# Performance work log

Hardware: AMD Instinct MI355X
Metric: run time of the kernel (lower is better)

The kernel has to match this reference:

```python
import jax, jax.numpy as jnp
import numpy as np

C = 16        # channel_n
HID = 128     # hidden width of 1x1 MLP
FIRE_RATE = 0.5
STEP_SIZE = 1.0
ALIVE_THRESH = 0.1
B, H, W = 16, 256, 256


def _perceive_kernel():
    # identity + Sobel filters, angle = 0.0 so cos=1, sin=0
    ident = np.outer([0.0, 1.0, 0.0], [0.0, 1.0, 0.0]).astype(np.float32)
    dxk = (np.outer([1.0, 2.0, 1.0], [-1.0, 0.0, 1.0]) / 8.0).astype(np.float32)
    dyk = dxk.T
    k3 = np.stack([ident, dxk, dyk], axis=-1)  # [3,3,3]
    # TF depthwise layout: out channel index = c*3 + k  -> tile over channels
    rhs = np.tile(k3, (1, 1, C)).reshape(3, 3, 1, 3 * C)  # HWIO, groups=C
    return jnp.asarray(rhs)


def _get_living_mask(x):
    alpha = x[:, :, :, 3:4]
    pooled = jax.lax.reduce_window(alpha, -jnp.inf, jax.lax.max,
                                   (1, 3, 3, 1), (1, 1, 1, 1), 'SAME')
    return pooled > ALIVE_THRESH


def _perceive(x):
    rhs = _perceive_kernel()
    return jax.lax.conv_general_dilated(
        x, rhs, window_strides=(1, 1), padding='SAME',
        dimension_numbers=('NHWC', 'HWIO', 'NHWC'),
        feature_group_count=C)  # [B,H,W,3C]


def setup_inputs() -> dict:
    key = jax.random.key(0)
    kx, kw1, kb1, ku = jax.random.split(key, 4)
    x = jax.random.normal(kx, (B, H, W, C), dtype=jnp.float32)
    # dmodel params: Conv2D(128,1,relu) then Conv2D(16,1,zeros init); use
    # random values for a meaningful numeric baseline
    W1 = jax.random.normal(kw1, (3 * C, HID), dtype=jnp.float32) * 0.1
    b1 = jax.random.normal(kb1, (HID,), dtype=jnp.float32) * 0.01
    W2 = jax.random.normal(jax.random.fold_in(key, 7), (HID, C), dtype=jnp.float32) * 0.1
    b2 = jnp.zeros((C,), dtype=jnp.float32)
    rand_u = jax.random.uniform(ku, (B, H, W, 1), dtype=jnp.float32)
    return {"x": x, "W1": W1, "b1": b1, "W2": W2, "b2": b2, "rand_u": rand_u}


def reference(x, W1, b1, W2, b2, rand_u):
    pre_life_mask = _get_living_mask(x)
    y = _perceive(x)                                         # [B,H,W,48]
    h = jax.nn.relu(jnp.einsum('bhwc,cd->bhwd', y, W1) + b1)  # [B,H,W,128]
    dx = (jnp.einsum('bhwd,dc->bhwc', h, W2) + b2) * STEP_SIZE
    update_mask = (rand_u <= FIRE_RATE).astype(x.dtype)
    x = x + dx * update_mask
    post_life_mask = _get_living_mask(x)
    life_mask = (pre_life_mask & post_life_mask).astype(x.dtype)
    return x * life_mask
```

## Files before the change

kernel.cpp:

```cpp
#include <hip/hip_runtime.h>


#define NC 16
#define NHID 128
#define NPIX (16 * 256 * 256)
#define MG 0.015f

typedef __attribute__((ext_vector_type(8))) short s8b;
typedef __attribute__((ext_vector_type(4))) float f4;

__device__ __forceinline__ unsigned short f2bf(float f) {
    union { float f; unsigned int u; } v; v.f = f;
    unsigned int r = (v.u + 0x7FFFu + ((v.u >> 16) & 1u)) >> 16;
    return (unsigned short)r;
}
__device__ __forceinline__ unsigned int pack2(float a, float b) {
    return (unsigned int)f2bf(a) | ((unsigned int)f2bf(b) << 16);
}

__global__ __launch_bounds__(256) void ca_prep(
    const float* __restrict__ W1, const float* __restrict__ b1,
    const float* __restrict__ W2, uint4* __restrict__ w1p, uint4* __restrict__ w2p)
{
    const int tid = threadIdx.x;
    if (blockIdx.x == 0) {
        for (int idx = tid; idx < 1024; idx += 256) {
            const int fid = idx >> 6, lane = idx & 63;
            const int k0 = fid >> 3, mt = fid & 7;
            const int q = lane >> 4, i = lane & 15;
            unsigned int u[4];
            #pragma unroll
            for (int jp = 0; jp < 4; ++jp) {
                int k = k0 * 32 + q * 8 + jp * 2;
                float v0 = (k < 48) ? W1[k * 128 + mt * 16 + i] : ((k == 48) ? b1[mt * 16 + i] : 0.f);
                k++;
                float v1 = (k < 48) ? W1[k * 128 + mt * 16 + i] : ((k == 48) ? b1[mt * 16 + i] : 0.f);
                u[jp] = pack2(v0, v1);
            }
            w1p[idx] = make_uint4(u[0], u[1], u[2], u[3]);
        }
    } else {
        for (int idx = tid; idx < 256; idx += 256) {
            const int k2 = idx >> 6, lane = idx & 63;
            const int q = lane >> 4, i = lane & 15;
            unsigned int u[4];
            #pragma unroll
            for (int jp = 0; jp < 4; ++jp) {
                const int k = k2 * 32 + q * 8 + jp * 2;
                u[jp] = pack2(W2[k * 16 + i], W2[(k + 1) * 16 + i]);
            }
            w2p[idx] = make_uint4(u[0], u[1], u[2], u[3]);
        }
    }
}

__global__ __launch_bounds__(256, 2) void ca_update(
    const float* __restrict__ x, const float* __restrict__ b2,
    const float* __restrict__ rand_u, const uint4* __restrict__ w1p,
    const uint4* __restrict__ w2p, float* __restrict__ out,
    float* __restrict__ ws_alpha, unsigned char* __restrict__ ws_pre)
{
    __shared__ __align__(16) float xt[18 * 18 * 20];
    __shared__ __align__(16) unsigned short yfs[4 * 2 * 528];
    __shared__ __align__(16) unsigned short hbs[4 * 16 * 136];
    __shared__ float lsr[256];

    const int tid  = threadIdx.x;
    const int lane = tid & 63;
    const int li   = lane & 15;
    const int lq   = lane >> 4;
    const int wv   = tid >> 6;
    const int tx   = tid & 15, ty = tid >> 4;
    const int w0 = blockIdx.x * 16, h0 = blockIdx.y * 16, bb = blockIdx.z;

    s8b w1f[2][8], w2f[4];
    const s8b* w1s = (const s8b*)w1p;
    const s8b* w2s = (const s8b*)w2p;
    #pragma unroll
    for (int k0 = 0; k0 < 2; ++k0)
        #pragma unroll
        for (int mt = 0; mt < 8; ++mt)
            w1f[k0][mt] = w1s[(k0 * 8 + mt) * 64 + lane];
    #pragma unroll
    for (int k2 = 0; k2 < 4; ++k2) w2f[k2] = w2s[k2 * 64 + lane];
    float b2v[4];
    #pragma unroll
    for (int r = 0; r < 4; ++r) b2v[r] = b2[lq * 4 + r];

    for (int i = tid; i < 324; i += 256) {
        const int ly = i / 18, lx = i - ly * 18;
        const int gh = h0 + ly - 1, gw = w0 + lx - 1;
        float4 v0, v1, v2, v3;
        if (gh >= 0 && gh < 256 && gw >= 0 && gw < 256) {
            const float4* p = (const float4*)(x + (((size_t)bb * 256 + gh) * 256 + gw) * NC);
            v0 = p[0]; v1 = p[1]; v2 = p[2]; v3 = p[3];
        } else {
            v0 = v1 = v2 = v3 = make_float4(0.f, 0.f, 0.f, 0.f);
        }
        float4* t = (float4*)(xt + i * 20);
        t[0] = v0; t[1] = v1; t[2] = v2; t[3] = v3;
    }
    const size_t gpix = ((size_t)bb * 256 + h0 + ty) * 256 + (w0 + tx);
    lsr[tid] = rand_u[gpix];
    __syncthreads();

    const int o_mm = ((ty + 0) * 18 + tx + 0) * 20, o_m0 = ((ty + 0) * 18 + tx + 1) * 20, o_mp = ((ty + 0) * 18 + tx + 2) * 20;
    const int o_0m = ((ty + 1) * 18 + tx + 0) * 20, o_cc = ((ty + 1) * 18 + tx + 1) * 20, o_0p = ((ty + 1) * 18 + tx + 2) * 20;
    const int o_pm = ((ty + 2) * 18 + tx + 0) * 20, o_p0 = ((ty + 2) * 18 + tx + 1) * 20, o_pp = ((ty + 2) * 18 + tx + 2) * 20;

    float am = xt[o_mm + 3];
    am = fmaxf(am, xt[o_m0 + 3]); am = fmaxf(am, xt[o_mp + 3]);
    am = fmaxf(am, xt[o_0m + 3]); am = fmaxf(am, xt[o_cc + 3]); am = fmaxf(am, xt[o_0p + 3]);
    am = fmaxf(am, xt[o_pm + 3]); am = fmaxf(am, xt[o_p0 + 3]); am = fmaxf(am, xt[o_pp + 3]);
    ws_pre[gpix] = (am > 0.1f) ? (unsigned char)1 : (unsigned char)0;

    unsigned int yu[24];
    #pragma unroll
    for (int cq = 0; cq < 4; ++cq) {
        const int co = cq * 4;
        float4 vmm = *(const float4*)(xt + o_mm + co); const float* pmm = (const float*)&vmm;
        float4 vm0 = *(const float4*)(xt + o_m0 + co); const float* pm0 = (const float*)&vm0;
        float4 vmp = *(const float4*)(xt + o_mp + co); const float* pmp = (const float*)&vmp;
        float4 v0m = *(const float4*)(xt + o_0m + co); const float* p0m = (const float*)&v0m;
        float4 vcc = *(const float4*)(xt + o_cc + co); const float* pcc = (const float*)&vcc;
        float4 v0p = *(const float4*)(xt + o_0p + co); const float* p0p = (const float*)&v0p;
        float4 vpm = *(const float4*)(xt + o_pm + co); const float* ppm = (const float*)&vpm;
        float4 vp0 = *(const float4*)(xt + o_p0 + co); const float* pp0 = (const float*)&vp0;
        float4 vpp = *(const float4*)(xt + o_pp + co); const float* ppp = (const float*)&vpp;
        float yl[12];
        #pragma unroll
        for (int cc = 0; cc < 4; ++cc) {
            const float xmm = pmm[cc], xm0 = pm0[cc], xmp = pmp[cc];
            const float x0m = p0m[cc], xcc = pcc[cc], x0p = p0p[cc];
            const float xpm = ppm[cc], xp0 = pp0[cc], xpp = ppp[cc];
            yl[cc * 3 + 0] = xcc;
            yl[cc * 3 + 1] = ((xmp - xmm) + 2.f * (x0p - x0m) + (xpp - xpm)) * 0.125f;
            yl[cc * 3 + 2] = ((xpm - xmm) + 2.f * (xp0 - xm0) + (xpp - xmp)) * 0.125f;
        }
        #pragma unroll
        for (int m2 = 0; m2 < 6; ++m2) yu[cq * 6 + m2] = pack2(yl[2 * m2], yl[2 * m2 + 1]);
    }

    unsigned short* yfw = yfs + wv * (2 * 528);
    unsigned short* hbw = hbs + wv * (16 * 136);

    for (int s = 0; s < 4; ++s) {
        const int t = wv * 4 + s;
        if ((ty & 3) == s) {
            #pragma unroll
            for (int q = 0; q < 4; ++q)
                *(uint4*)(yfw + (q * 16 + tx) * 8) = make_uint4(yu[q * 4], yu[q * 4 + 1], yu[q * 4 + 2], yu[q * 4 + 3]);
            *(uint4*)(yfw + 528 + (0 * 16 + tx) * 8) = make_uint4(yu[16], yu[17], yu[18], yu[19]);
            *(uint4*)(yfw + 528 + (1 * 16 + tx) * 8) = make_uint4(yu[20], yu[21], yu[22], yu[23]);
            *(uint4*)(yfw + 528 + (2 * 16 + tx) * 8) = make_uint4(0x3F80u, 0u, 0u, 0u);
            *(uint4*)(yfw + 528 + (3 * 16 + tx) * 8) = make_uint4(0u, 0u, 0u, 0u);
        }
        __syncthreads();
        const s8b ya0 = *(const s8b*)(yfw + lane * 8);
        const s8b ya1 = *(const s8b*)(yfw + 528 + lane * 8);
        f4 acc1[8];
        #pragma unroll
        for (int mt = 0; mt < 8; ++mt) { f4 z = {0.f, 0.f, 0.f, 0.f}; acc1[mt] = z; }
        #pragma unroll
        for (int mt = 0; mt < 8; ++mt)
            acc1[mt] = __builtin_amdgcn_mfma_f32_16x16x32_bf16(w1f[0][mt], ya0, acc1[mt], 0, 0, 0);
        #pragma unroll
        for (int mt = 0; mt < 8; ++mt)
            acc1[mt] = __builtin_amdgcn_mfma_f32_16x16x32_bf16(w1f[1][mt], ya1, acc1[mt], 0, 0, 0);
        #pragma unroll
        for (int mt = 0; mt < 8; ++mt) {
            const float hh0 = fmaxf(acc1[mt][0], 0.f), hh1 = fmaxf(acc1[mt][1], 0.f);
            const float hh2 = fmaxf(acc1[mt][2], 0.f), hh3 = fmaxf(acc1[mt][3], 0.f);
            *(uint2*)(hbw + li * 136 + mt * 16 + lq * 4) = make_uint2(pack2(hh0, hh1), pack2(hh2, hh3));
        }
        __syncthreads();
        f4 acc2 = {0.f, 0.f, 0.f, 0.f};
        #pragma unroll
        for (int k2 = 0; k2 < 4; ++k2) {
            const s8b hf = *(const s8b*)(hbw + li * 136 + k2 * 32 + lq * 8);
            acc2 = __builtin_amdgcn_mfma_f32_16x16x32_bf16(w2f[k2], hf, acc2, 0, 0, 0);
        }
        const float um = (lsr[t * 16 + li] <= 0.5f) ? 1.f : 0.f;
        const float4 xc = *(const float4*)(xt + ((t + 1) * 18 + li + 1) * 20 + lq * 4);
        float4 nx;
        nx.x = fmaf(acc2[0] + b2v[0], um, xc.x);
        nx.y = fmaf(acc2[1] + b2v[1], um, xc.y);
        nx.z = fmaf(acc2[2] + b2v[2], um, xc.z);
        nx.w = fmaf(acc2[3] + b2v[3], um, xc.w);
        const size_t gp = ((size_t)bb * 256 + h0 + t) * 256 + (w0 + li);
        ((float4*)out)[gp * 4 + lq] = nx;
        if (lq == 0) ws_alpha[gp] = nx.w;
    }
}

__device__ float exact_alpha(
    const float* __restrict__ x, const float* __restrict__ W1,
    const float* __restrict__ b1, const float* __restrict__ W2,
    const float* __restrict__ b2, const float* __restrict__ rand_u,
    int bb, int gh, int gw)
{
    const size_t p = ((size_t)bb * 256 + gh) * 256 + gw;
    const float xa = x[p * 16 + 3];
    if (rand_u[p] > 0.5f) return xa;
    float y[48];
    #pragma unroll
    for (int k = 0; k < 48; ++k) y[k] = 0.f;
    for (int dy = 0; dy < 3; ++dy) {
        for (int dx = 0; dx < 3; ++dx) {
            const int hh = gh + dy - 1, ww = gw + dx - 1;
            if (hh < 0 || hh >= 256 || ww < 0 || ww >= 256) continue;
            const float* f = x + (((size_t)bb * 256 + hh) * 256 + ww) * 16;
            const float rw = (dy == 1) ? 2.f : 1.f;
            const float cw = (dx == 1) ? 2.f : 1.f;
            const float wx = rw * (float)(dx - 1) * 0.125f;
            const float wy = cw * (float)(dy - 1) * 0.125f;
            const bool ctr = (dy == 1 && dx == 1);
            #pragma unroll
            for (int c = 0; c < 16; ++c) {
                const float v = f[c];
                if (ctr) y[3 * c] = v;
                y[3 * c + 1] = fmaf(v, wx, y[3 * c + 1]);
                y[3 * c + 2] = fmaf(v, wy, y[3 * c + 2]);
            }
        }
    }
    float dot = b2[3];
    for (int d4 = 0; d4 < 32; ++d4) {
        const float4 a4 = *(const float4*)(b1 + d4 * 4);
        float a0 = a4.x, a1 = a4.y, a2 = a4.z, a3 = a4.w;
        for (int k = 0; k < 48; ++k) {
            const float4 w = *(const float4*)(W1 + k * 128 + d4 * 4);
            const float yk = y[k];
            a0 = fmaf(yk, w.x, a0); a1 = fmaf(yk, w.y, a1);
            a2 = fmaf(yk, w.z, a2); a3 = fmaf(yk, w.w, a3);
        }
        dot = fmaf(fmaxf(a0, 0.f), W2[(d4 * 4 + 0) * 16 + 3], dot);
        dot = fmaf(fmaxf(a1, 0.f), W2[(d4 * 4 + 1) * 16 + 3], dot);
        dot = fmaf(fmaxf(a2, 0.f), W2[(d4 * 4 + 2) * 16 + 3], dot);
        dot = fmaf(fmaxf(a3, 0.f), W2[(d4 * 4 + 3) * 16 + 3], dot);
    }
    return xa + dot;
}

__global__ __launch_bounds__(256) void ca_mask(
    const float* __restrict__ x, const float* __restrict__ W1,
    const float* __restrict__ b1, const float* __restrict__ W2,
    const float* __restrict__ b2, const float* __restrict__ rand_u,
    const float* __restrict__ alpha, const unsigned char* __restrict__ pre,
    float* __restrict__ out)
{
    __shared__ float at[18 * 20];
    const int tid = threadIdx.x;
    const int w0 = blockIdx.x * 16, h0 = blockIdx.y * 16, bb = blockIdx.z;
    for (int i = tid; i < 324; i += 256) {
        const int ly = i / 18, lx = i - ly * 18;
        const int gh = h0 + ly - 1, gw = w0 + lx - 1;
        float v = 0.f;
        if (gh >= 0 && gh < 256 && gw >= 0 && gw < 256)
            v = alpha[((size_t)bb * 256 + gh) * 256 + gw];
        at[ly * 20 + lx] = v;
    }
    __syncthreads();
    const int txx = tid & 15, tyy = tid >> 4;
    float m = at[tyy * 20 + txx];
    m = fmaxf(m, at[tyy * 20 + txx + 1]); m = fmaxf(m, at[tyy * 20 + txx + 2]);
    m = fmaxf(m, at[(tyy + 1) * 20 + txx]); m = fmaxf(m, at[(tyy + 1) * 20 + txx + 1]); m = fmaxf(m, at[(tyy + 1) * 20 + txx + 2]);
    m = fmaxf(m, at[(tyy + 2) * 20 + txx]); m = fmaxf(m, at[(tyy + 2) * 20 + txx + 1]); m = fmaxf(m, at[(tyy + 2) * 20 + txx + 2]);
    bool alive;
    if (m > 0.1f + MG) alive = true;
    else if (m <= 0.1f - MG) alive = false;
    else {
        alive = false;
        for (int nb = 0; nb < 9; ++nb) {
            if (alive) break;
            const int dy = nb / 3, dx = nb - dy * 3;
            const float a = at[(tyy + dy) * 20 + txx + dx];
            if (a > 0.1f - MG) {
                const float tr = exact_alpha(x, W1, b1, W2, b2, rand_u, bb, h0 + tyy + dy - 1, w0 + txx + dx - 1);
                if (tr > 0.1f) alive = true;
            }
        }
    }
    const size_t gp = ((size_t)bb * 256 + h0 + tyy) * 256 + (w0 + txx);
    const float sc = (alive && pre[gp]) ? 1.f : 0.f;
    float4* po = (float4*)(out + gp * 16);
    #pragma unroll
    for (int i2 = 0; i2 < 4; ++i2) {
        float4 v = po[i2]; v.x *= sc; v.y *= sc; v.z *= sc; v.w *= sc; po[i2] = v;
    }
}

extern "C" void kernel_launch(void* const* d_in, const int* in_sizes, int n_in,
                              void* d_out, int out_size, void* d_ws, size_t ws_size,
                              hipStream_t stream) {
    (void)in_sizes; (void)n_in; (void)out_size; (void)ws_size;
    const float* x  = (const float*)d_in[0];
    const float* W1 = (const float*)d_in[1];
    const float* b1 = (const float*)d_in[2];
    const float* W2 = (const float*)d_in[3];
    const float* b2 = (const float*)d_in[4];
    const float* ru = (const float*)d_in[5];
    float* out = (float*)d_out;
    float* ws_alpha = (float*)d_ws;
    unsigned char* ws_pre = (unsigned char*)(ws_alpha + NPIX);
    uint4* w1p = (uint4*)((char*)d_ws + (size_t)NPIX * 5);
    uint4* w2p = w1p + 1024;

    ca_prep<<<2, 256, 0, stream>>>(W1, b1, W2, w1p, w2p);
    dim3 g(16, 16, 16);
    ca_update<<<g, 256, 0, stream>>>(x, b2, ru, w1p, w2p, out, ws_alpha, ws_pre);
    ca_mask<<<g, 256, 0, stream>>>(x, W1, b1, W2, b2, ru, ws_alpha, ws_pre, out);
}
```

Before: 340.0 us.

## Move near-threshold alpha recomputation into a compacted fix-list kernel

The update kernel now appends pixels whose bf16-computed alpha lies near the alive threshold to a global list via atomics. A new ca_fix kernel recomputes exact fp32 alpha for those pixels with one wavefront per pixel, so the mask kernel reduces to a plain max-pool that only zeroes dead pixels. This replaces the divergent per-thread exact recompute inside the mask kernel. Two __syncthreads in the update loop are also dropped, since each wave uses only its own LDS slice. The list is capped at MAXFIX, so overflow would silently skip corrections, and the wider margin produces more fix entries.

```diff
diff --git a/kernel.cpp b/kernel.cpp
--- a/kernel.cpp
+++ b/kernel.cpp
@@ -4,7 +4,8 @@
 #define NC 16
 #define NHID 128
 #define NPIX (16 * 256 * 256)
-#define MG 0.015f
+#define MG 0.04f
+#define MAXFIX 65536
 
 typedef __attribute__((ext_vector_type(8))) short s8b;
 typedef __attribute__((ext_vector_type(4))) float f4;
@@ -58,7 +59,8 @@
     const float* __restrict__ x, const float* __restrict__ b2,
     const float* __restrict__ rand_u, const uint4* __restrict__ w1p,
     const uint4* __restrict__ w2p, float* __restrict__ out,
-    float* __restrict__ ws_alpha, unsigned char* __restrict__ ws_pre)
+    float* __restrict__ ws_alpha, unsigned char* __restrict__ ws_pre,
+    unsigned int* __restrict__ fix_cnt, unsigned int* __restrict__ fix_list)
 {
     __shared__ __align__(16) float xt[18 * 18 * 20];
     __shared__ __align__(16) unsigned short yfs[4 * 2 * 528];
@@ -155,7 +157,6 @@
             *(uint4*)(yfw + 528 + (2 * 16 + tx) * 8) = make_uint4(0x3F80u, 0u, 0u, 0u);
             *(uint4*)(yfw + 528 + (3 * 16 + tx) * 8) = make_uint4(0u, 0u, 0u, 0u);
         }
-        __syncthreads();
         const s8b ya0 = *(const s8b*)(yfw + lane * 8);
         const s8b ya1 = *(const s8b*)(yfw + 528 + lane * 8);
         f4 acc1[8];
@@ -173,7 +174,6 @@
             const float hh2 = fmaxf(acc1[mt][2], 0.f), hh3 = fmaxf(acc1[mt][3], 0.f);
             *(uint2*)(hbw + li * 136 + mt * 16 + lq * 4) = make_uint2(pack2(hh0, hh1), pack2(hh2, hh3));
         }
-        __syncthreads();
         f4 acc2 = {0.f, 0.f, 0.f, 0.f};
         #pragma unroll
         for (int k2 = 0; k2 < 4; ++k2) {
@@ -189,63 +189,70 @@
         nx.w = fmaf(acc2[3] + b2v[3], um, xc.w);
         const size_t gp = ((size_t)bb * 256 + h0 + t) * 256 + (w0 + li);
         ((float4*)out)[gp * 4 + lq] = nx;
-        if (lq == 0) ws_alpha[gp] = nx.w;
-    }
-}
-
-__device__ float exact_alpha(
+        if (lq == 0) {
+            ws_alpha[gp] = nx.w;
+            if (um != 0.f && fabsf(nx.w - 0.1f) <= MG) {
+                unsigned int idx = atomicAdd(fix_cnt, 1u);
+                if (idx < MAXFIX) fix_list[idx] = (unsigned int)gp;
+            }
+        }
+    }
+}
+
+__global__ __launch_bounds__(64) void ca_fix(
     const float* __restrict__ x, const float* __restrict__ W1,
     const float* __restrict__ b1, const float* __restrict__ W2,
-    const float* __restrict__ b2, const float* __restrict__ rand_u,
-    int bb, int gh, int gw)
+    const float* __restrict__ b2,
+    const unsigned int* __restrict__ fix_cnt, const unsigned int* __restrict__ fix_list,
+    float* __restrict__ ws_alpha)
 {
-    const size_t p = ((size_t)bb * 256 + gh) * 256 + gw;
-    const float xa = x[p * 16 + 3];
-    if (rand_u[p] > 0.5f) return xa;
-    float y[48];
-    #pragma unroll
-    for (int k = 0; k < 48; ++k) y[k] = 0.f;
-    for (int dy = 0; dy < 3; ++dy) {
-        for (int dx = 0; dx < 3; ++dx) {
-            const int hh = gh + dy - 1, ww = gw + dx - 1;
-            if (hh < 0 || hh >= 256 || ww < 0 || ww >= 256) continue;
-            const float* f = x + (((size_t)bb * 256 + hh) * 256 + ww) * 16;
-            const float rw = (dy == 1) ? 2.f : 1.f;
-            const float cw = (dx == 1) ? 2.f : 1.f;
-            const float wx = rw * (float)(dx - 1) * 0.125f;
-            const float wy = cw * (float)(dy - 1) * 0.125f;
-            const bool ctr = (dy == 1 && dx == 1);
-            #pragma unroll
-            for (int c = 0; c < 16; ++c) {
-                const float v = f[c];
-                if (ctr) y[3 * c] = v;
-                y[3 * c + 1] = fmaf(v, wx, y[3 * c + 1]);
-                y[3 * c + 2] = fmaf(v, wy, y[3 * c + 2]);
+    __shared__ float ysh[48];
+    const int lane = threadIdx.x;
+    unsigned int n = *fix_cnt;
+    if (n > MAXFIX) n = MAXFIX;
+    for (unsigned int e = blockIdx.x; e < n; e += gridDim.x) {
+        const unsigned int pix = fix_list[e];
+        const int bb = pix >> 16, h = (pix >> 8) & 255, w = pix & 255;
+        if (lane < 48) {
+            const int c = lane / 3, j = lane - c * 3;
+            float v = 0.f;
+            #pragma unroll
+            for (int dy = 0; dy < 3; ++dy) {
+                #pragma unroll
+                for (int dxx = 0; dxx < 3; ++dxx) {
+                    const int hh = h + dy - 1, ww = w + dxx - 1;
+                    if (hh < 0 || hh >= 256 || ww < 0 || ww >= 256) continue;
+                    const float f = x[(((size_t)bb * 256 + hh) * 256 + ww) * 16 + c];
+                    float wgt;
+                    if (j == 0) wgt = (dy == 1 && dxx == 1) ? 1.f : 0.f;
+                    else if (j == 1) wgt = ((dy == 1) ? 2.f : 1.f) * (float)(dxx - 1) * 0.125f;
+                    else wgt = ((dxx == 1) ? 2.f : 1.f) * (float)(dy - 1) * 0.125f;
+                    v = fmaf(f, wgt, v);
+                }
             }
-        }
-    }
-    float dot = b2[3];
-    for (int d4 = 0; d4 < 32; ++d4) {
-        const float4 a4 = *(const float4*)(b1 + d4 * 4);
-        float a0 = a4.x, a1 = a4.y, a2 = a4.z, a3 = a4.w;
-        for (int k = 0; k < 48; ++k) {
-            const float4 w = *(const float4*)(W1 + k * 128 + d4 * 4);
-            const float yk = y[k];
-            a0 = fmaf(yk, w.x, a0); a1 = fmaf(yk, w.y, a1);
-            a2 = fmaf(yk, w.z, a2); a3 = fmaf(yk, w.w, a3);
-        }
-        dot = fmaf(fmaxf(a0, 0.f), W2[(d4 * 4 + 0) * 16 + 3], dot);
-        dot = fmaf(fmaxf(a1, 0.f), W2[(d4 * 4 + 1) * 16 + 3], dot);
-        dot = fmaf(fmaxf(a2, 0.f), W2[(d4 * 4 + 2) * 16 + 3], dot);
-        dot = fmaf(fmaxf(a3, 0.f), W2[(d4 * 4 + 3) * 16 + 3], dot);
-    }
-    return xa + dot;
+            ysh[lane] = v;
+        }
+        __syncthreads();
+        float dot = 0.f;
+        #pragma unroll
+        for (int t = 0; t < 2; ++t) {
+            const int d = t * 64 + lane;
+            float a = b1[d];
+            #pragma unroll
+            for (int k = 0; k < 48; ++k)
+                a = fmaf(ysh[k], W1[k * 128 + d], a);
+            dot = fmaf(fmaxf(a, 0.f), W2[d * 16 + 3], dot);
+        }
+        #pragma unroll
+        for (int off = 32; off > 0; off >>= 1)
+            dot += __shfl_down(dot, off, 64);
+        if (lane == 0)
+            ws_alpha[pix] = x[(size_t)pix * 16 + 3] + dot + b2[3];
+        __syncthreads();
+    }
 }
 
 __global__ __launch_bounds__(256) void ca_mask(
-    const float* __restrict__ x, const float* __restrict__ W1,
-    const float* __restrict__ b1, const float* __restrict__ W2,
-    const float* __restrict__ b2, const float* __restrict__ rand_u,
     const float* __restrict__ alpha, const unsigned char* __restrict__ pre,
     float* __restrict__ out)
 {
@@ -266,27 +273,12 @@
     m = fmaxf(m, at[tyy * 20 + txx + 1]); m = fmaxf(m, at[tyy * 20 + txx + 2]);
     m = fmaxf(m, at[(tyy + 1) * 20 + txx]); m = fmaxf(m, at[(tyy + 1) * 20 + txx + 1]); m = fmaxf(m, at[(tyy + 1) * 20 + txx + 2]);
     m = fmaxf(m, at[(tyy + 2) * 20 + txx]); m = fmaxf(m, at[(tyy + 2) * 20 + txx + 1]); m = fmaxf(m, at[(tyy + 2) * 20 + txx + 2]);
-    bool alive;
-    if (m > 0.1f + MG) alive = true;
-    else if (m <= 0.1f - MG) alive = false;
-    else {
-        alive = false;
-        for (int nb = 0; nb < 9; ++nb) {
-            if (alive) break;
-            const int dy = nb / 3, dx = nb - dy * 3;
-            const float a = at[(tyy + dy) * 20 + txx + dx];
-            if (a > 0.1f - MG) {
-                const float tr = exact_alpha(x, W1, b1, W2, b2, rand_u, bb, h0 + tyy + dy - 1, w0 + txx + dx - 1);
-                if (tr > 0.1f) alive = true;
-            }
-        }
-    }
     const size_t gp = ((size_t)bb * 256 + h0 + tyy) * 256 + (w0 + txx);
-    const float sc = (alive && pre[gp]) ? 1.f : 0.f;
-    float4* po = (float4*)(out + gp * 16);
-    #pragma unroll
-    for (int i2 = 0; i2 < 4; ++i2) {
-        float4 v = po[i2]; v.x *= sc; v.y *= sc; v.z *= sc; v.w *= sc; po[i2] = v;
+    const bool alive = (m > 0.1f) && pre[gp];
+    if (!alive) {
+        float4* po = (float4*)(out + gp * 16);
+        const float4 z = make_float4(0.f, 0.f, 0.f, 0.f);
+        po[0] = z; po[1] = z; po[2] = z; po[3] = z;
     }
 }
 
@@ -301,13 +293,19 @@
     const float* b2 = (const float*)d_in[4];
     const float* ru = (const float*)d_in[5];
     float* out = (float*)d_out;
-    float* ws_alpha = (float*)d_ws;
-    unsigned char* ws_pre = (unsigned char*)(ws_alpha + NPIX);
-    uint4* w1p = (uint4*)((char*)d_ws + (size_t)NPIX * 5);
-    uint4* w2p = w1p + 1024;
-
+
+    char* ws = (char*)d_ws;
+    float* ws_alpha       = (float*)ws;
+    unsigned char* ws_pre = (unsigned char*)(ws + (size_t)NPIX * 4);
+    uint4* w1p            = (uint4*)(ws + (size_t)NPIX * 5);
+    uint4* w2p            = w1p + 1024;
+    unsigned int* fix_cnt = (unsigned int*)(ws + (size_t)NPIX * 5 + 20480);
+    unsigned int* fix_list= fix_cnt + 4;
+
+    hipMemsetAsync(fix_cnt, 0, sizeof(unsigned int), stream);
     ca_prep<<<2, 256, 0, stream>>>(W1, b1, W2, w1p, w2p);
     dim3 g(16, 16, 16);
-    ca_update<<<g, 256, 0, stream>>>(x, b2, ru, w1p, w2p, out, ws_alpha, ws_pre);
-    ca_mask<<<g, 256, 0, stream>>>(x, W1, b1, W2, b2, ru, ws_alpha, ws_pre, out);
-}
+    ca_update<<<g, 256, 0, stream>>>(x, b2, ru, w1p, w2p, out, ws_alpha, ws_pre, fix_cnt, fix_list);
+    ca_fix<<<4096, 64, 0, stream>>>(x, W1, b1, W2, b2, fix_cnt, fix_list, ws_alpha);
+    ca_mask<<<g, 256, 0, stream>>>(ws_alpha, ws_pre, out);
+}
```

Result: faster. 332.8 us (-2.1%).
